# Kernel tuning notes

Measured on AMD Instinct MI355X. Metric: run time of the kernel, lower is better.

The kernel has to match this reference:

```python
import jax, jax.numpy as jnp
import numpy as np

B, S, D_MODEL, H, D_KV, D_FF = 2, 2048, 1024, 16, 64, 4096
NUM_BUCKETS, MAX_DISTANCE = 32, 128
EPS = 1e-6


def rms_norm(x, w, eps=EPS):
    var = jnp.mean(jnp.square(x), axis=-1, keepdims=True)
    return x * jax.lax.rsqrt(var + eps) * w


def gelu_new(x):
    c = np.sqrt(2.0 / np.pi).astype(np.float32)
    return 0.5 * x * (1.0 + jnp.tanh(c * (x + 0.044715 * x * x * x)))


def rel_position_bucket(qlen, klen, num_buckets=NUM_BUCKETS, max_distance=MAX_DISTANCE):
    # bidirectional (encoder) T5 bucketing
    ctx = jnp.arange(qlen)[:, None]
    mem = jnp.arange(klen)[None, :]
    rel = mem - ctx  # [q, k]
    nb = num_buckets // 2
    ret = (rel > 0).astype(jnp.int32) * nb
    n = jnp.abs(rel)
    max_exact = nb // 2
    is_small = n < max_exact
    val_large = max_exact + (
        jnp.log(jnp.maximum(n, 1).astype(jnp.float32) / max_exact)
        / np.log(max_distance / max_exact) * (nb - max_exact)
    ).astype(jnp.int32)
    val_large = jnp.minimum(val_large, nb - 1)
    return ret + jnp.where(is_small, n, val_large)


def setup_inputs() -> dict:
    key = jax.random.key(0)
    ks = jax.random.split(key, 12)
    sd = 1.0 / np.sqrt(D_MODEL)
    sf = 1.0 / np.sqrt(D_FF)
    return {
        "hidden_states": jax.random.normal(ks[0], (B, S, D_MODEL), jnp.float32),
        "attention_mask": jnp.ones((B, S), jnp.float32),
        "ln1_w": jnp.ones((D_MODEL,), jnp.float32),
        "wq": jax.random.normal(ks[1], (D_MODEL, H * D_KV), jnp.float32) * sd,
        "wk": jax.random.normal(ks[2], (D_MODEL, H * D_KV), jnp.float32) * sd,
        "wv": jax.random.normal(ks[3], (D_MODEL, H * D_KV), jnp.float32) * sd,
        "rel_bias": jax.random.normal(ks[4], (NUM_BUCKETS, H), jnp.float32) * 0.5,
        "wo": jax.random.normal(ks[5], (H * D_KV, D_MODEL), jnp.float32) * sd,
        "ln2_w": jnp.ones((D_MODEL,), jnp.float32),
        "w1": jax.random.normal(ks[6], (D_MODEL, D_FF), jnp.float32) * sd,
        "w2": jax.random.normal(ks[7], (D_MODEL, D_FF), jnp.float32) * sd,
        "w_out": jax.random.normal(ks[8], (D_FF, D_MODEL), jnp.float32) * sf,
    }


def reference(hidden_states, attention_mask, ln1_w, wq, wk, wv, rel_bias, wo,
              ln2_w, w1, w2, w_out):
    b, s, _ = hidden_states.shape
    # --- self attention (pre-LN) ---
    normed = rms_norm(hidden_states, ln1_w)
    q = (normed @ wq).reshape(b, s, H, D_KV)
    k = (normed @ wk).reshape(b, s, H, D_KV)
    v = (normed @ wv).reshape(b, s, H, D_KV)
    scores = jnp.einsum('bqhd,bkhd->bhqk', q, k)  # no 1/sqrt(d) scaling (T5)
    buckets = rel_position_bucket(s, s)            # [q, k] int32
    bias = rel_bias[buckets]                       # [q, k, H]
    scores = scores + jnp.transpose(bias, (2, 0, 1))[None]
    mask_add = (1.0 - attention_mask)[:, None, None, :] * -10000.0
    probs = jax.nn.softmax(scores + mask_add, axis=-1)
    ctx = jnp.einsum('bhqk,bkhd->bqhd', probs, v).reshape(b, s, H * D_KV)
    hidden = hidden_states + ctx @ wo
    # --- gated FFN (pre-LN) ---
    normed2 = rms_norm(hidden, ln2_w)
    ff = (gelu_new(normed2 @ w1) * (normed2 @ w2)) @ w_out
    return hidden + ff
```

## Files before the change

kernel.cpp:

```cpp
#include <hip/hip_runtime.h>
#include <math.h>

typedef unsigned short u16;
typedef unsigned int u32;
typedef __attribute__((ext_vector_type(8))) short short8;
typedef __attribute__((ext_vector_type(4))) float f32x4;

__device__ __forceinline__ float b2f(u16 u) {
    u32 x = ((u32)u) << 16;
    return __builtin_bit_cast(float, x);
}
__device__ __forceinline__ u16 f2b(float f) {
    u32 x = __builtin_bit_cast(u32, f);
    u32 r = x + 0x7fffu + ((x >> 16) & 1u);
    return (u16)(r >> 16);
}
__device__ __forceinline__ void split_hl(float x, u16& h, u16& l) {
    u16 hb = f2b(x);
    h = hb;
    l = f2b(x - b2f(hb));
}
__device__ __forceinline__ float gelu_new_f(float x) {
    const float c = 0.7978845608028654f;
    float y = c * (x + 0.044715f * x * x * x);
    float t = 1.0f - 2.0f / (1.0f + __expf(2.0f * y));
    return 0.5f * x * (1.0f + t);
}
__device__ __forceinline__ float scrub(float v, float s) {
    return (fabsf(v) < 1e25f) ? v : s;
}
__device__ __forceinline__ void gld16(const void* g, void* l) {
    __builtin_amdgcn_global_load_lds((const __attribute__((address_space(1))) u32*)g,
                                     (__attribute__((address_space(3))) u32*)l,
                                     16, 0, 0);
}
__device__ __forceinline__ short8 ldf(const u16* p) { return *(const short8*)p; }

__global__ __launch_bounds__(256) void transpose_cvt(const float* __restrict__ src,
                                                     u16* __restrict__ dst, int R, int C) {
    __shared__ u16 t[32][33];
    int c0 = blockIdx.x * 32, r0 = blockIdx.y * 32;
    int x = threadIdx.x & 31, y = threadIdx.x >> 5;
#pragma unroll
    for (int i = 0; i < 32; i += 8)
        t[y + i][x] = f2b(src[(size_t)(r0 + y + i) * C + c0 + x]);
    __syncthreads();
#pragma unroll
    for (int i = 0; i < 32; i += 8)
        dst[(size_t)(c0 + y + i) * R + r0 + x] = t[x][y + i];
}

__global__ void bias_table_kernel(const float* __restrict__ rel_bias,
                                  const float* __restrict__ mask,
                                  float* __restrict__ tab,
                                  float* __restrict__ mask_add) {
    const float LOG2E = 1.4426950408889634f;
    int idx = blockIdx.x * 256 + threadIdx.x;
    if (idx < 4095) {
        int rel = idx - 2047;
        int ret = rel > 0 ? 16 : 0;
        int n = rel < 0 ? -rel : rel;
        int bucket;
        if (n < 8) {
            bucket = ret + n;
        } else {
            int v = 8 + (int)(logf((float)n * 0.125f) * (8.0f / 2.7725887222397811f));
            v = v < 15 ? v : 15;
            bucket = ret + v;
        }
#pragma unroll
        for (int h = 0; h < 16; h++)
            tab[h * 4096 + idx] = rel_bias[bucket * 16 + h] * LOG2E;
    }
    if (idx < 4096)
        mask_add[idx] = ((1.0f - mask[idx]) * -10000.0f - 20.0f) * LOG2E;
}

__global__ __launch_bounds__(256) void rmsnorm_k(const float* __restrict__ X,
                                                 const float* __restrict__ W,
                                                 u16* __restrict__ Y) {
    __shared__ float red[4];
    int row = blockIdx.x, tid = threadIdx.x;
    const float* xr = X + (size_t)row * 1024;
    float4 x = *(const float4*)(xr + tid * 4);
    float ss = x.x * x.x + x.y * x.y + x.z * x.z + x.w * x.w;
#pragma unroll
    for (int off = 32; off; off >>= 1) ss += __shfl_xor(ss, off, 64);
    if ((tid & 63) == 0) red[tid >> 6] = ss;
    __syncthreads();
    float tot = red[0] + red[1] + red[2] + red[3];
    float s = rsqrtf(tot * (1.0f / 1024.0f) + 1e-6f);
    float4 w4 = *(const float4*)(W + tid * 4);
    float y0 = scrub(x.x * s * w4.x, 1e3f);
    float y1 = scrub(x.y * s * w4.y, 1e3f);
    float y2 = scrub(x.z * s * w4.z, 1e3f);
    float y3 = scrub(x.w * s * w4.w, 1e3f);
    uint2 o;
    o.x = (u32)f2b(y0) | ((u32)f2b(y1) << 16);
    o.y = (u32)f2b(y2) | ((u32)f2b(y3) << 16);
    *(uint2*)(Y + (size_t)row * 1024 + tid * 4) = o;
}


__global__ __launch_bounds__(256) void gemm_qkv(const u16* __restrict__ A,
                                                const u16* __restrict__ Bt,
                                                float* __restrict__ qb,
                                                u16* __restrict__ Kh,
                                                u16* __restrict__ Kl,
                                                u16* __restrict__ vT) {
    const int K = 1024;
    __shared__ __align__(16) u16 As[128 * 64];
    __shared__ __align__(16) u16 Bs[128 * 64];
    int tid = threadIdx.x;
    int wave = tid >> 6, lane = tid & 63, quad = lane >> 4, l15 = lane & 15;
    int bm = blockIdx.y * 128, bn = blockIdx.x * 128;
    int wm = (wave >> 1) * 64, wn = (wave & 1) * 64;
    f32x4 acc[4][4] = {};
    int lr = lane >> 3, cb = (lane & 7) ^ (lr & 7);
    const u16* ga = A + (size_t)(bm + wave * 32 + lr) * K + cb * 8;
    const u16* gb = Bt + (size_t)(bn + wave * 32 + lr) * K + cb * 8;
    u16* la = As + wave * 2048;
    u16* lb = Bs + wave * 2048;
    int swz = l15 & 7;
    for (int k0 = 0; k0 < K; k0 += 64) {
        __syncthreads();
#pragma unroll
        for (int g = 0; g < 4; g++) {
            gld16(ga + k0 + (size_t)(g * 8) * K, la + g * 512);
            gld16(gb + k0 + (size_t)(g * 8) * K, lb + g * 512);
        }
        __syncthreads();
#pragma unroll
        for (int s = 0; s < 2; s++) {
            int kb = ((s * 4 + quad) ^ swz) * 8;
            short8 af[4], bf[4];
#pragma unroll
            for (int i = 0; i < 4; i++)
                af[i] = ldf(As + (wm + i * 16 + l15) * 64 + kb);
#pragma unroll
            for (int j = 0; j < 4; j++)
                bf[j] = ldf(Bs + (wn + j * 16 + l15) * 64 + kb);
#pragma unroll
            for (int i = 0; i < 4; i++)
#pragma unroll
                for (int j = 0; j < 4; j++)
                    acc[i][j] = __builtin_amdgcn_mfma_f32_16x16x32_bf16(af[i], bf[j], acc[i][j], 0, 0, 0);
        }
    }
    if (bn < 1024) {
#pragma unroll
        for (int i = 0; i < 4; i++)
#pragma unroll
            for (int j = 0; j < 4; j++) {
                int col = bn + wn + j * 16 + l15;
#pragma unroll
                for (int r = 0; r < 4; r++) {
                    int row = bm + wm + i * 16 + quad * 4 + r;
                    qb[(size_t)row * 1024 + col] = scrub(acc[i][j][r], 1e4f);
                }
            }
    } else if (bn < 2048) {
#pragma unroll
        for (int i = 0; i < 4; i++)
#pragma unroll
            for (int j = 0; j < 4; j++) {
                int col = bn - 1024 + wn + j * 16 + l15;
#pragma unroll
                for (int r = 0; r < 4; r++) {
                    int row = bm + wm + i * 16 + quad * 4 + r;
                    u16 hh, ll;
                    split_hl(scrub(acc[i][j][r], 1e4f), hh, ll);
                    Kh[(size_t)row * 1024 + col] = hh;
                    Kl[(size_t)row * 1024 + col] = ll;
                }
            }
    } else {
#pragma unroll
        for (int i = 0; i < 4; i++)
#pragma unroll
            for (int j = 0; j < 4; j++) {
                int col = bn - 2048 + wn + j * 16 + l15;
                int row0 = bm + wm + i * 16 + quad * 4;
                ushort4 p;
                p.x = f2b(scrub(acc[i][j][0], 1e4f));
                p.y = f2b(scrub(acc[i][j][1], 1e4f));
                p.z = f2b(scrub(acc[i][j][2], 1e4f));
                p.w = f2b(scrub(acc[i][j][3], 1e4f));
                *(ushort4*)(vT + (size_t)col * 4096 + row0) = p;
            }
    }
}

__global__ __launch_bounds__(256) void gemm_bt_res(const u16* __restrict__ A,
                                                   const u16* __restrict__ Bt,
                                                   float* __restrict__ C,
                                                   const float* __restrict__ Res,
                                                   int M, int N, int K, float sval) {
    __shared__ __align__(16) u16 As[128 * 64];
    __shared__ __align__(16) u16 Bs[128 * 64];
    int tid = threadIdx.x;
    int wave = tid >> 6, lane = tid & 63, quad = lane >> 4, l15 = lane & 15;
    int bm = blockIdx.y * 128, bn = blockIdx.x * 128;
    int wm = (wave >> 1) * 64, wn = (wave & 1) * 64;
    f32x4 acc[4][4] = {};
    int lr = lane >> 3, cb = (lane & 7) ^ (lr & 7);
    const u16* ga = A + (size_t)(bm + wave * 32 + lr) * K + cb * 8;
    const u16* gb = Bt + (size_t)(bn + wave * 32 + lr) * K + cb * 8;
    u16* la = As + wave * 2048;
    u16* lb = Bs + wave * 2048;
    int swz = l15 & 7;
    for (int k0 = 0; k0 < K; k0 += 64) {
        __syncthreads();
#pragma unroll
        for (int g = 0; g < 4; g++) {
            gld16(ga + k0 + (size_t)(g * 8) * K, la + g * 512);
            gld16(gb + k0 + (size_t)(g * 8) * K, lb + g * 512);
        }
        __syncthreads();
#pragma unroll
        for (int s = 0; s < 2; s++) {
            int kb = ((s * 4 + quad) ^ swz) * 8;
            short8 af[4], bf[4];
#pragma unroll
            for (int i = 0; i < 4; i++)
                af[i] = ldf(As + (wm + i * 16 + l15) * 64 + kb);
#pragma unroll
            for (int j = 0; j < 4; j++)
                bf[j] = ldf(Bs + (wn + j * 16 + l15) * 64 + kb);
#pragma unroll
            for (int i = 0; i < 4; i++)
#pragma unroll
                for (int j = 0; j < 4; j++)
                    acc[i][j] = __builtin_amdgcn_mfma_f32_16x16x32_bf16(af[i], bf[j], acc[i][j], 0, 0, 0);
        }
    }
#pragma unroll
    for (int i = 0; i < 4; i++)
#pragma unroll
        for (int j = 0; j < 4; j++) {
            int col = bn + wn + j * 16 + l15;
#pragma unroll
            for (int r = 0; r < 4; r++) {
                int row = bm + wm + i * 16 + quad * 4 + r;
                float v = acc[i][j][r] + Res[(size_t)row * N + col];
                C[(size_t)row * N + col] = scrub(v, sval);
            }
        }
}

__global__ __launch_bounds__(256) void gemm_dual_gelu(const u16* __restrict__ A,
                                                      const u16* __restrict__ B1t,
                                                      const u16* __restrict__ B2t,
                                                      u16* __restrict__ C,
                                                      int M, int N, int K) {
    __shared__ __align__(16) u16 As[256 * 64];
    __shared__ __align__(16) u16 B1s[128 * 64];
    __shared__ __align__(16) u16 B2s[128 * 64];
    int tid = threadIdx.x;
    int wave = tid >> 6, lane = tid & 63, quad = lane >> 4, l15 = lane & 15;
    int bm = blockIdx.y * 256, bn = blockIdx.x * 128;
    int wm = (wave >> 1) * 128, wn = (wave & 1) * 64;
    f32x4 acc1[8][4] = {};
    f32x4 acc2[8][4] = {};
    int lr = lane >> 3, cb = (lane & 7) ^ (lr & 7);
    const u16* ga = A + (size_t)(bm + wave * 64 + lr) * K + cb * 8;
    const u16* g1 = B1t + (size_t)(bn + wave * 32 + lr) * K + cb * 8;
    const u16* g2 = B2t + (size_t)(bn + wave * 32 + lr) * K + cb * 8;
    u16* la = As + wave * 4096;
    u16* l1 = B1s + wave * 2048;
    u16* l2 = B2s + wave * 2048;
    int swz = l15 & 7;
    for (int k0 = 0; k0 < K; k0 += 64) {
        __syncthreads();
#pragma unroll
        for (int g = 0; g < 8; g++)
            gld16(ga + k0 + (size_t)(g * 8) * K, la + g * 512);
#pragma unroll
        for (int g = 0; g < 4; g++) {
            gld16(g1 + k0 + (size_t)(g * 8) * K, l1 + g * 512);
            gld16(g2 + k0 + (size_t)(g * 8) * K, l2 + g * 512);
        }
        __syncthreads();
#pragma unroll
        for (int s = 0; s < 2; s++) {
            int kb = ((s * 4 + quad) ^ swz) * 8;
            short8 b1f[4], b2f_[4];
#pragma unroll
            for (int j = 0; j < 4; j++) {
                b1f[j] = ldf(B1s + (wn + j * 16 + l15) * 64 + kb);
                b2f_[j] = ldf(B2s + (wn + j * 16 + l15) * 64 + kb);
            }
#pragma unroll
            for (int i = 0; i < 8; i++) {
                short8 af = ldf(As + (wm + i * 16 + l15) * 64 + kb);
#pragma unroll
                for (int j = 0; j < 4; j++) {
                    acc1[i][j] = __builtin_amdgcn_mfma_f32_16x16x32_bf16(af, b1f[j], acc1[i][j], 0, 0, 0);
                    acc2[i][j] = __builtin_amdgcn_mfma_f32_16x16x32_bf16(af, b2f_[j], acc2[i][j], 0, 0, 0);
                }
            }
        }
    }
#pragma unroll
    for (int i = 0; i < 8; i++)
#pragma unroll
        for (int j = 0; j < 4; j++) {
            int col = bn + wn + j * 16 + l15;
#pragma unroll
            for (int r = 0; r < 4; r++) {
                int row = bm + wm + i * 16 + quad * 4 + r;
                float v = gelu_new_f(acc1[i][j][r]) * acc2[i][j][r];
                C[(size_t)row * N + col] = f2b(scrub(v, 1e10f));
            }
        }
}

__global__ __launch_bounds__(256) void attn_kernel(const float* __restrict__ Qb,
                                                   const u16* __restrict__ Kh,
                                                   const u16* __restrict__ Kl,
                                                   const u16* __restrict__ vT,
                                                   const float* __restrict__ bias_tab,
                                                   const float* __restrict__ mask_add,
                                                   u16* __restrict__ Ctx) {
    __shared__ __align__(16) u16 Khs[64 * 64];
    __shared__ __align__(16) u16 Kls[64 * 64];
    __shared__ __align__(16) u16 Vs[64 * 64];
    __shared__ __align__(16) u16 Pss[4 * 16 * 72];
    const float LOG2E = 1.4426950408889634f;
    int tid = threadIdx.x, wave = tid >> 6, lane = tid & 63;
    int quad = lane >> 4, l15 = lane & 15;
    int h = blockIdx.y, b = blockIdx.z;
    int q0 = blockIdx.x * 64;
    short8 qh0, qh1, ql0, ql1;
    {
        const float* Qg = Qb + (size_t)(b * 2048 + q0 + wave * 16 + l15) * 1024 + h * 64 + quad * 8;
#pragma unroll
        for (int half = 0; half < 2; half++) {
            float4 a = *(const float4*)(Qg + half * 32);
            float4 c = *(const float4*)(Qg + half * 32 + 4);
            u16 hh, ll;
            float vals[8] = {a.x, a.y, a.z, a.w, c.x, c.y, c.z, c.w};
#pragma unroll
            for (int j = 0; j < 8; j++) {
                split_hl(vals[j] * LOG2E, hh, ll);
                if (half == 0) { qh0[j] = (short)hh; ql0[j] = (short)ll; }
                else           { qh1[j] = (short)hh; ql1[j] = (short)ll; }
            }
        }
    }
    f32x4 O[4] = {};
    f32x4 O4 = {};
    short8 vones;
#pragma unroll
    for (int i = 0; i < 8; i++) vones[i] = (short)0x3f80;
    u16* Pw = Pss + wave * 16 * 72;
    int my_q = q0 + wave * 16 + quad * 4;
    const float* bt = bias_tab + h * 4096;
    const float* ma = mask_add + b * 2048;
    float bsat_neg = bt[0];
    float bsat_pos = bt[4094];
    int lr8 = lane >> 3, cb = (lane & 7) ^ (lr8 & 7);
    const u16* gkh = Kh + (size_t)(b * 2048 + wave * 16 + lr8) * 1024 + h * 64 + cb * 8;
    const u16* gkl = Kl + (size_t)(b * 2048 + wave * 16 + lr8) * 1024 + h * 64 + cb * 8;
    const u16* gv  = vT + (size_t)(h * 64 + wave * 16 + lr8) * 4096 + b * 2048 + cb * 8;
    u16* lkh = Khs + wave * 1024;
    u16* lkl = Kls + wave * 1024;
    u16* lv  = Vs + wave * 1024;
    int sw = l15 & 7;
    int swK0 = (quad ^ sw) * 8, swK1 = ((quad + 4) ^ sw) * 8;

    for (int k0 = 0; k0 < 2048; k0 += 64) {
        __syncthreads();
        gld16(gkh + (size_t)k0 * 1024, lkh);
        gld16(gkh + (size_t)k0 * 1024 + 8 * 1024, lkh + 512);
        gld16(gkl + (size_t)k0 * 1024, lkl);
        gld16(gkl + (size_t)k0 * 1024 + 8 * 1024, lkl + 512);
        gld16(gv + k0, lv);
        gld16(gv + k0 + (size_t)8 * 4096, lv + 512);
        __syncthreads();
        float pv[4][4];
        int dq = k0 - q0;
        if (dq >= 192 || dq <= -192) {
            float bsat = dq > 0 ? bsat_pos : bsat_neg;
#pragma unroll
            for (int t = 0; t < 4; t++) {
                const u16* krow = Khs + (t * 16 + l15) * 64;
                const u16* lrow = Kls + (t * 16 + l15) * 64;
                short8 kh0 = ldf(krow + swK0);
                short8 kh1 = ldf(krow + swK1);
                short8 kl0 = ldf(lrow + swK0);
                short8 kl1 = ldf(lrow + swK1);
                f32x4 z = {0.0f, 0.0f, 0.0f, 0.0f};
                z = __builtin_amdgcn_mfma_f32_16x16x32_bf16(ql0, kh0, z, 0, 0, 0);
                z = __builtin_amdgcn_mfma_f32_16x16x32_bf16(ql1, kh1, z, 0, 0, 0);
                z = __builtin_amdgcn_mfma_f32_16x16x32_bf16(qh0, kl0, z, 0, 0, 0);
                z = __builtin_amdgcn_mfma_f32_16x16x32_bf16(qh1, kl1, z, 0, 0, 0);
                z = __builtin_amdgcn_mfma_f32_16x16x32_bf16(qh0, kh0, z, 0, 0, 0);
                z = __builtin_amdgcn_mfma_f32_16x16x32_bf16(qh1, kh1, z, 0, 0, 0);
                float c = ma[k0 + t * 16 + l15] + bsat;
#pragma unroll
                for (int r = 0; r < 4; r++)
                    pv[t][r] = exp2f(z[r] + c);
            }
        } else {
#pragma unroll
            for (int t = 0; t < 4; t++) {
                const u16* krow = Khs + (t * 16 + l15) * 64;
                const u16* lrow = Kls + (t * 16 + l15) * 64;
                short8 kh0 = ldf(krow + swK0);
                short8 kh1 = ldf(krow + swK1);
                short8 kl0 = ldf(lrow + swK0);
                short8 kl1 = ldf(lrow + swK1);
                f32x4 z = {0.0f, 0.0f, 0.0f, 0.0f};
                z = __builtin_amdgcn_mfma_f32_16x16x32_bf16(ql0, kh0, z, 0, 0, 0);
                z = __builtin_amdgcn_mfma_f32_16x16x32_bf16(ql1, kh1, z, 0, 0, 0);
                z = __builtin_amdgcn_mfma_f32_16x16x32_bf16(qh0, kl0, z, 0, 0, 0);
                z = __builtin_amdgcn_mfma_f32_16x16x32_bf16(qh1, kl1, z, 0, 0, 0);
                z = __builtin_amdgcn_mfma_f32_16x16x32_bf16(qh0, kh0, z, 0, 0, 0);
                z = __builtin_amdgcn_mfma_f32_16x16x32_bf16(qh1, kh1, z, 0, 0, 0);
                int kcol = k0 + t * 16 + l15;
                float madd = ma[kcol];
#pragma unroll
                for (int r = 0; r < 4; r++)
                    pv[t][r] = exp2f(z[r] + bt[kcol - (my_q + r) + 2047] + madd);
            }
        }
#pragma unroll
        for (int t = 0; t < 4; t++)
#pragma unroll
            for (int r = 0; r < 4; r++)
                Pw[(quad * 4 + r) * 72 + t * 16 + l15] = f2b(pv[t][r]);
#pragma unroll
        for (int h2 = 0; h2 < 2; h2++) {
            short8 pf = ldf(Pw + l15 * 72 + h2 * 32 + quad * 8);
#pragma unroll
            for (int nt = 0; nt < 4; nt++) {
                short8 vf = ldf(Vs + (nt * 16 + l15) * 64 + ((h2 * 4 + quad) ^ sw) * 8);
                O[nt] = __builtin_amdgcn_mfma_f32_16x16x32_bf16(pf, vf, O[nt], 0, 0, 0);
            }
            O4 = __builtin_amdgcn_mfma_f32_16x16x32_bf16(pf, vones, O4, 0, 0, 0);
        }
    }
    u16* Cg = Ctx + ((size_t)(b * 2048 + my_q)) * 1024 + h * 64;
#pragma unroll
    for (int nt = 0; nt < 4; nt++)
#pragma unroll
        for (int r = 0; r < 4; r++) {
            float v = O[nt][r] / fmaxf(O4[r], 1e-30f);
            Cg[(size_t)r * 1024 + nt * 16 + l15] = f2b(scrub(v, 1e6f));
        }
}

extern "C" void kernel_launch(void* const* d_in, const int* in_sizes, int n_in,
                              void* d_out, int out_size, void* d_ws, size_t ws_size,
                              hipStream_t stream) {
    const float* hidden = (const float*)d_in[0];
    const float* mask   = (const float*)d_in[1];
    const float* ln1_w  = (const float*)d_in[2];
    const float* wq     = (const float*)d_in[3];
    const float* wk     = (const float*)d_in[4];
    const float* wv     = (const float*)d_in[5];
    const float* relb   = (const float*)d_in[6];
    const float* wo     = (const float*)d_in[7];
    const float* ln2_w  = (const float*)d_in[8];
    const float* w1     = (const float*)d_in[9];
    const float* w2     = (const float*)d_in[10];
    const float* w_out  = (const float*)d_in[11];
    float* out = (float*)d_out;

    char* w = (char*)d_ws;
    const size_t MB = 1u << 20;
    u16*   qkvT    = (u16*)(w + 0 * MB);
    u16*   woutT   = (u16*)(w + 0 * MB);
    u16*   woT     = (u16*)(w + 6 * MB);
    u16*   w1T     = (u16*)(w + 8 * MB);
    u16*   w2T     = (u16*)(w + 16 * MB);
    u16*   normed  = (u16*)(w + 24 * MB);
    u16*   ctx     = (u16*)(w + 24 * MB);
    u16*   normed2 = (u16*)(w + 24 * MB);
    u16*   Kh      = (u16*)(w + 40 * MB);
    u16*   Kl      = (u16*)(w + 48 * MB);
    u16*   vT      = (u16*)(w + 56 * MB);
    u16*   ffg     = (u16*)(w + 32 * MB);
    float* bias_tab = (float*)(w + 64 * MB);
    float* mask_add = (float*)(w + 64 * MB + 256 * 1024);
    float* qb      = (float*)d_out;

    dim3 blk(256);
    transpose_cvt<<<dim3(32, 32), blk, 0, stream>>>(wq, qkvT, 1024, 1024);
    transpose_cvt<<<dim3(32, 32), blk, 0, stream>>>(wk, qkvT + 1024 * 1024, 1024, 1024);
    transpose_cvt<<<dim3(32, 32), blk, 0, stream>>>(wv, qkvT + 2048 * 1024, 1024, 1024);
    transpose_cvt<<<dim3(32, 32), blk, 0, stream>>>(wo, woT, 1024, 1024);
    transpose_cvt<<<dim3(128, 32), blk, 0, stream>>>(w1, w1T, 1024, 4096);
    transpose_cvt<<<dim3(128, 32), blk, 0, stream>>>(w2, w2T, 1024, 4096);
    bias_table_kernel<<<16, 256, 0, stream>>>(relb, mask, bias_tab, mask_add);

    rmsnorm_k<<<4096, blk, 0, stream>>>(hidden, ln1_w, normed);
    gemm_qkv<<<dim3(24, 32), blk, 0, stream>>>(normed, qkvT, qb, Kh, Kl, vT);

    attn_kernel<<<dim3(32, 16, 2), blk, 0, stream>>>(qb, Kh, Kl, vT, bias_tab, mask_add, ctx);

    gemm_bt_res<<<dim3(8, 32), blk, 0, stream>>>(ctx, woT, out, hidden, 4096, 1024, 1024, 1e8f);

    transpose_cvt<<<dim3(32, 128), blk, 0, stream>>>(w_out, woutT, 4096, 1024);

    rmsnorm_k<<<4096, blk, 0, stream>>>(out, ln2_w, normed2);
    gemm_dual_gelu<<<dim3(32, 16), blk, 0, stream>>>(normed2, w1T, w2T, ffg, 4096, 4096, 1024);
    gemm_bt_res<<<dim3(8, 32), blk, 0, stream>>>(ffg, woutT, out, out, 4096, 1024, 4096, 1e12f);
}
```

Baseline: 506.6 us.

## Merge weight prep into one kernel and split-K the output GEMMs with atomics

Seven transpose/convert launches plus the bias-table launch become a single prep kernel using 64x64 tiles with float4 loads, and the w_out transpose moves into it. The two residual GEMMs become split-K kernels (2 and 4 slices) that atomically add into an output pre-seeded with the residual via a device memcpy, raising block count for the 256-tile grids. This drops the scrub clamping of outputs, adds atomic traffic and makes summation order nondeterministic.

```diff
diff --git a/kernel.cpp b/kernel.cpp
--- a/kernel.cpp
+++ b/kernel.cpp
@@ -36,44 +36,68 @@
 }
 __device__ __forceinline__ short8 ldf(const u16* p) { return *(const short8*)p; }
 
-__global__ __launch_bounds__(256) void transpose_cvt(const float* __restrict__ src,
-                                                     u16* __restrict__ dst, int R, int C) {
-    __shared__ u16 t[32][33];
-    int c0 = blockIdx.x * 32, r0 = blockIdx.y * 32;
-    int x = threadIdx.x & 31, y = threadIdx.x >> 5;
-#pragma unroll
-    for (int i = 0; i < 32; i += 8)
-        t[y + i][x] = f2b(src[(size_t)(r0 + y + i) * C + c0 + x]);
+__global__ __launch_bounds__(256) void prep_kernel(
+        const float* __restrict__ wq, const float* __restrict__ wk,
+        const float* __restrict__ wv, const float* __restrict__ wo,
+        const float* __restrict__ w1, const float* __restrict__ w2,
+        const float* __restrict__ w_out,
+        const float* __restrict__ rel_bias, const float* __restrict__ mask,
+        u16* __restrict__ qkvT, u16* __restrict__ woT,
+        u16* __restrict__ w1T, u16* __restrict__ w2T, u16* __restrict__ woutT,
+        float* __restrict__ tab, float* __restrict__ mask_add) {
+    int bid = blockIdx.x, tid = threadIdx.x;
+    if (bid >= 4096) {
+        const float LOG2E = 1.4426950408889634f;
+        int idx = (bid - 4096) * 256 + tid;
+        if (idx < 4095) {
+            int rel = idx - 2047;
+            int ret = rel > 0 ? 16 : 0;
+            int n = rel < 0 ? -rel : rel;
+            int bucket;
+            if (n < 8) {
+                bucket = ret + n;
+            } else {
+                int v = 8 + (int)(logf((float)n * 0.125f) * (8.0f / 2.7725887222397811f));
+                v = v < 15 ? v : 15;
+                bucket = ret + v;
+            }
+#pragma unroll
+            for (int h = 0; h < 16; h++)
+                tab[h * 4096 + idx] = rel_bias[bucket * 16 + h] * LOG2E;
+        }
+        if (idx < 4096)
+            mask_add[idx] = ((1.0f - mask[idx]) * -10000.0f - 20.0f) * LOG2E;
+        return;
+    }
+    const float* src; u16* dst; int R, C, tile;
+    if (bid < 1024) {
+        int m = bid >> 8; tile = bid & 255; R = 1024; C = 1024;
+        src = (m == 0) ? wq : (m == 1) ? wk : (m == 2) ? wv : wo;
+        dst = (m < 3) ? qkvT + (size_t)m * 1024 * 1024 : woT;
+    } else if (bid < 2048) { tile = bid - 1024; src = w1; dst = w1T; R = 1024; C = 4096; }
+    else if (bid < 3072)   { tile = bid - 2048; src = w2; dst = w2T; R = 1024; C = 4096; }
+    else                   { tile = bid - 3072; src = w_out; dst = woutT; R = 4096; C = 1024; }
+    int tc = C >> 6;
+    int r0 = (tile / tc) * 64, c0 = (tile % tc) * 64;
+    __shared__ u16 t[64][68];
+    int x = tid & 15, y = tid >> 4;
+#pragma unroll
+    for (int i = 0; i < 64; i += 16) {
+        float4 v = *(const float4*)(src + (size_t)(r0 + y + i) * C + c0 + x * 4);
+        ushort4 p;
+        p.x = f2b(v.x); p.y = f2b(v.y); p.z = f2b(v.z); p.w = f2b(v.w);
+        *(ushort4*)&t[y + i][x * 4] = p;
+    }
     __syncthreads();
 #pragma unroll
-    for (int i = 0; i < 32; i += 8)
-        dst[(size_t)(c0 + y + i) * R + r0 + x] = t[x][y + i];
-}
-
-__global__ void bias_table_kernel(const float* __restrict__ rel_bias,
-                                  const float* __restrict__ mask,
-                                  float* __restrict__ tab,
-                                  float* __restrict__ mask_add) {
-    const float LOG2E = 1.4426950408889634f;
-    int idx = blockIdx.x * 256 + threadIdx.x;
-    if (idx < 4095) {
-        int rel = idx - 2047;
-        int ret = rel > 0 ? 16 : 0;
-        int n = rel < 0 ? -rel : rel;
-        int bucket;
-        if (n < 8) {
-            bucket = ret + n;
-        } else {
-            int v = 8 + (int)(logf((float)n * 0.125f) * (8.0f / 2.7725887222397811f));
-            v = v < 15 ? v : 15;
-            bucket = ret + v;
-        }
-#pragma unroll
-        for (int h = 0; h < 16; h++)
-            tab[h * 4096 + idx] = rel_bias[bucket * 16 + h] * LOG2E;
-    }
-    if (idx < 4096)
-        mask_add[idx] = ((1.0f - mask[idx]) * -10000.0f - 20.0f) * LOG2E;
+    for (int i = 0; i < 64; i += 16) {
+        ushort4 p;
+        p.x = t[x * 4 + 0][y + i];
+        p.y = t[x * 4 + 1][y + i];
+        p.z = t[x * 4 + 2][y + i];
+        p.w = t[x * 4 + 3][y + i];
+        *(ushort4*)(dst + (size_t)(c0 + y + i) * R + r0 + x * 4) = p;
+    }
 }
 
 __global__ __launch_bounds__(256) void rmsnorm_k(const float* __restrict__ X,
@@ -191,25 +215,26 @@
     }
 }
 
-__global__ __launch_bounds__(256) void gemm_bt_res(const u16* __restrict__ A,
-                                                   const u16* __restrict__ Bt,
-                                                   float* __restrict__ C,
-                                                   const float* __restrict__ Res,
-                                                   int M, int N, int K, float sval) {
+template <int SPLITK>
+__global__ __launch_bounds__(256) void gemm_bt_atomic(const u16* __restrict__ A,
+                                                      const u16* __restrict__ Bt,
+                                                      float* __restrict__ C,
+                                                      int M, int N, int K) {
     __shared__ __align__(16) u16 As[128 * 64];
     __shared__ __align__(16) u16 Bs[128 * 64];
     int tid = threadIdx.x;
     int wave = tid >> 6, lane = tid & 63, quad = lane >> 4, l15 = lane & 15;
     int bm = blockIdx.y * 128, bn = blockIdx.x * 128;
     int wm = (wave >> 1) * 64, wn = (wave & 1) * 64;
+    int kslice = K / SPLITK, kbeg = blockIdx.z * kslice;
     f32x4 acc[4][4] = {};
     int lr = lane >> 3, cb = (lane & 7) ^ (lr & 7);
-    const u16* ga = A + (size_t)(bm + wave * 32 + lr) * K + cb * 8;
-    const u16* gb = Bt + (size_t)(bn + wave * 32 + lr) * K + cb * 8;
+    const u16* ga = A + (size_t)(bm + wave * 32 + lr) * K + kbeg + cb * 8;
+    const u16* gb = Bt + (size_t)(bn + wave * 32 + lr) * K + kbeg + cb * 8;
     u16* la = As + wave * 2048;
     u16* lb = Bs + wave * 2048;
     int swz = l15 & 7;
-    for (int k0 = 0; k0 < K; k0 += 64) {
+    for (int k0 = 0; k0 < kslice; k0 += 64) {
         __syncthreads();
 #pragma unroll
         for (int g = 0; g < 4; g++) {
@@ -242,8 +267,7 @@
 #pragma unroll
             for (int r = 0; r < 4; r++) {
                 int row = bm + wm + i * 16 + quad * 4 + r;
-                float v = acc[i][j][r] + Res[(size_t)row * N + col];
-                C[(size_t)row * N + col] = scrub(v, sval);
+                unsafeAtomicAdd(&C[(size_t)row * N + col], acc[i][j][r]);
             }
         }
 }
@@ -471,7 +495,6 @@
     char* w = (char*)d_ws;
     const size_t MB = 1u << 20;
     u16*   qkvT    = (u16*)(w + 0 * MB);
-    u16*   woutT   = (u16*)(w + 0 * MB);
     u16*   woT     = (u16*)(w + 6 * MB);
     u16*   w1T     = (u16*)(w + 8 * MB);
     u16*   w2T     = (u16*)(w + 16 * MB);
@@ -484,27 +507,22 @@
     u16*   ffg     = (u16*)(w + 32 * MB);
     float* bias_tab = (float*)(w + 64 * MB);
     float* mask_add = (float*)(w + 64 * MB + 256 * 1024);
+    u16*   woutT   = (u16*)(w + 65 * MB);
     float* qb      = (float*)d_out;
 
     dim3 blk(256);
-    transpose_cvt<<<dim3(32, 32), blk, 0, stream>>>(wq, qkvT, 1024, 1024);
-    transpose_cvt<<<dim3(32, 32), blk, 0, stream>>>(wk, qkvT + 1024 * 1024, 1024, 1024);
-    transpose_cvt<<<dim3(32, 32), blk, 0, stream>>>(wv, qkvT + 2048 * 1024, 1024, 1024);
-    transpose_cvt<<<dim3(32, 32), blk, 0, stream>>>(wo, woT, 1024, 1024);
-    transpose_cvt<<<dim3(128, 32), blk, 0, stream>>>(w1, w1T, 1024, 4096);
-    transpose_cvt<<<dim3(128, 32), blk, 0, stream>>>(w2, w2T, 1024, 4096);
-    bias_table_kernel<<<16, 256, 0, stream>>>(relb, mask, bias_tab, mask_add);
+    prep_kernel<<<4112, blk, 0, stream>>>(wq, wk, wv, wo, w1, w2, w_out, relb, mask,
+                                          qkvT, woT, w1T, w2T, woutT, bias_tab, mask_add);
 
     rmsnorm_k<<<4096, blk, 0, stream>>>(hidden, ln1_w, normed);
     gemm_qkv<<<dim3(24, 32), blk, 0, stream>>>(normed, qkvT, qb, Kh, Kl, vT);
 
     attn_kernel<<<dim3(32, 16, 2), blk, 0, stream>>>(qb, Kh, Kl, vT, bias_tab, mask_add, ctx);
 
-    gemm_bt_res<<<dim3(8, 32), blk, 0, stream>>>(ctx, woT, out, hidden, 4096, 1024, 1024, 1e8f);
-
-    transpose_cvt<<<dim3(32, 128), blk, 0, stream>>>(w_out, woutT, 4096, 1024);
+    hipMemcpyAsync(out, hidden, (size_t)4096 * 1024 * 4, hipMemcpyDeviceToDevice, stream);
+    gemm_bt_atomic<2><<<dim3(8, 32, 2), blk, 0, stream>>>(ctx, woT, out, 4096, 1024, 1024);
 
     rmsnorm_k<<<4096, blk, 0, stream>>>(out, ln2_w, normed2);
     gemm_dual_gelu<<<dim3(32, 16), blk, 0, stream>>>(normed2, w1T, w2T, ffg, 4096, 4096, 1024);
-    gemm_bt_res<<<dim3(8, 32), blk, 0, stream>>>(ffg, woutT, out, out, 4096, 1024, 4096, 1e12f);
-}
+    gemm_bt_atomic<4><<<dim3(8, 32, 4), blk, 0, stream>>>(ffg, woutT, out, 4096, 1024, 4096);
+}
```

New measurement: 516.8 us. Within noise of the previous version (+2.0%).
